# Performance work log

Hardware: AMD Instinct MI355X
Metric: run time of the kernel (lower is better)

Reference implementation:

```python
import jax, jax.numpy as jnp
import numpy as np

N = 500000
M = 8  # max vertices after clipping a 4-gon by 4 half-planes


def _angle_sort(q):
    # q: (4,2) points in convex position -> CCW-ordered convex quad (== convex hull)
    c = q.mean(axis=0)
    ang = jnp.arctan2(q[:, 1] - c[1], q[:, 0] - c[0])
    return q[jnp.argsort(ang)]


def _poly_inter_area(subj, clip):
    # Sutherland-Hodgman clipping of CCW convex quad `subj` by CCW convex quad `clip`.
    poly = jnp.zeros((M, 2), subj.dtype).at[:4].set(subj)
    n = jnp.array(4, jnp.int32)
    edges = jnp.stack([clip, jnp.roll(clip, -1, axis=0)], axis=1)  # (4,2,2)

    def clip_edge(state, edge):
        poly, n = state
        a, b = edge[0], edge[1]
        e = b - a
        idx = jnp.arange(M)
        n_safe = jnp.maximum(n, 1)
        nxt = poly[(idx + 1) % n_safe]
        d_cur = e[0] * (poly[:, 1] - a[1]) - e[1] * (poly[:, 0] - a[0])
        d_nxt = e[0] * (nxt[:, 1] - a[1]) - e[1] * (nxt[:, 0] - a[0])
        in_cur = d_cur >= 0
        in_nxt = d_nxt >= 0
        den = d_cur - d_nxt
        den = jnp.where(jnp.abs(den) < 1e-12, 1e-12, den)
        t = (d_cur / den)[:, None]
        ipt = poly + t * (nxt - poly)
        active = idx < n
        pts = jnp.stack([poly, ipt], axis=1).reshape(2 * M, 2)
        valid = jnp.stack([active & in_cur, active & (in_cur != in_nxt)], axis=1).reshape(2 * M)
        pos = jnp.cumsum(valid) - 1
        new_poly = jnp.zeros((M, 2), poly.dtype).at[jnp.where(valid, pos, M)].set(pts, mode='drop')
        return (new_poly, jnp.sum(valid).astype(jnp.int32)), None

    (poly, n), _ = jax.lax.scan(clip_edge, (poly, n), edges)
    idx = jnp.arange(M)
    n_safe = jnp.maximum(n, 1)
    nxtv = poly[(idx + 1) % n_safe]
    mask = (idx < n).astype(poly.dtype)
    return 0.5 * jnp.abs(jnp.sum(mask * (poly[:, 0] * nxtv[:, 1] - nxtv[:, 0] * poly[:, 1])))


def _hull_area8(pts):
    # Area of convex hull of 8 points via gift wrapping (fixed 8 steps, pads by repeating start).
    P = 8
    start = jnp.argmin(pts[:, 1]).astype(jnp.int32)

    def next_idx(cur):
        rel = pts - pts[cur]
        d2 = jnp.sum(rel * rel, axis=1)
        C = rel[:, 0, None] * rel[None, :, 1] - rel[:, 1, None] * rel[None, :, 0]  # C[j,k]=cross(rel_j, rel_k)
        valid = jnp.all(C >= -1e-6, axis=1) & (d2 > 1e-12)  # all points left of cur->j
        score = jnp.where(valid, d2, -1.0)
        return jnp.argmax(score).astype(jnp.int32)

    def step(carry, _):
        cur, done = carry
        nxt = next_idx(cur)
        nxt = jnp.where(done, cur, nxt)
        done = done | (nxt == start)
        return (nxt, done), nxt

    _, seq = jax.lax.scan(step, (start, jnp.array(False)), None, length=P)
    order = jnp.concatenate([start[None], seq])  # (9,)
    v = pts[order]
    x, y = v[:, 0], v[:, 1]
    xn, yn = jnp.roll(x, -1), jnp.roll(y, -1)
    return 0.5 * jnp.abs(jnp.sum(x * yn - xn * y))


def _pair_loss(pred8, tgt8):
    p = _angle_sort(pred8.reshape(4, 2))
    t = _angle_sort(tgt8.reshape(4, 2))
    inter = _poly_inter_area(p, t)
    hull = _hull_area8(jnp.concatenate([p, t], axis=0))  # convex hull of union of points
    iou = jnp.where(hull > 1e-12, inter / jnp.maximum(hull, 1e-12), 0.0)
    return 1.0 - iou  # reduction='none', loss_type='iou'


def setup_inputs() -> dict:
    key = jax.random.key(0)
    ks = jax.random.split(key, 6)

    def make_quads(ka, kb, kc):
        # 4 vertices in convex position: sorted angles + radius in [0.5, 1.5]
        ang = jnp.sort(jax.random.uniform(ka, (N, 4)) * (2.0 * np.pi), axis=1)
        rad = 0.5 + jax.random.uniform(kb, (N, 4))
        ctr = jax.random.normal(kc, (N, 1, 2)) * 0.5
        pts = ctr + jnp.stack([rad * jnp.cos(ang), rad * jnp.sin(ang)], axis=-1)
        return pts.reshape(N, 8).astype(jnp.float32)

    preds = make_quads(ks[0], ks[1], ks[2])
    targets = make_quads(ks[3], ks[4], ks[5])
    return {"preds": preds, "targets": targets}


def reference(preds, targets):
    return jax.vmap(_pair_loss)(preds, targets)
```

## Files before the change

### kernel.cpp

```cpp
#include <hip/hip_runtime.h>
#include <math.h>

struct V2 { float x, y; };

#define NT 256

__device__ __forceinline__ int ang_class(float x, float y) {
    return (y < 0.f) ? 0 : ((y > 0.f) ? 2 : ((x >= 0.f) ? 1 : 3));
}

__device__ __forceinline__ void angle_sort4(float4 lo, float4 hi, V2 out[4]) {
    V2 p[4];
    p[0].x = lo.x; p[0].y = lo.y;
    p[1].x = lo.z; p[1].y = lo.w;
    p[2].x = hi.x; p[2].y = hi.y;
    p[3].x = hi.z; p[3].y = hi.w;
    float cx = (((p[0].x + p[1].x) + p[2].x) + p[3].x) * 0.25f;
    float cy = (((p[0].y + p[1].y) + p[2].y) + p[3].y) * 0.25f;
    float rx[4], ry[4]; int cls[4];
#pragma unroll
    for (int i = 0; i < 4; i++) {
        rx[i] = p[i].x - cx; ry[i] = p[i].y - cy;
        cls[i] = ang_class(rx[i], ry[i]);
    }
    int rank[4] = {0, 0, 0, 0};
#pragma unroll
    for (int i = 0; i < 4; i++) {
#pragma unroll
        for (int j = i + 1; j < 4; j++) {
            int cd = cls[i] - cls[j];
            double cr = (double)rx[i] * (double)ry[j] - (double)ry[i] * (double)rx[j];
            bool gt = (cd > 0) || (cd == 0 && cr < 0.0);
            rank[i] += gt ? 1 : 0;
            rank[j] += gt ? 0 : 1;
        }
    }
#pragma unroll
    for (int k = 0; k < 4; k++) {
#pragma unroll
        for (int i = 0; i < 4; i++) {
            if (rank[i] == k) out[k] = p[i];
        }
    }
}

__device__ __forceinline__ int clip_mid(float2 (*buf)[NT], V2 A, V2 B,
                                        int nv, int tid)
{
    float ex = B.x - A.x, ey = B.y - A.y;
    V2 p[8]; float d[8];
#pragma unroll
    for (int s = 0; s < 8; s++) {
        float2 v = buf[s][tid];
        p[s].x = v.x; p[s].y = v.y;
        d[s] = ex * (v.y - A.y) - ey * (v.x - A.x);
    }
    int cnt = 0;
#pragma unroll
    for (int idx = 0; idx < 8; idx++) {
        V2 nx; float dn;
        if (idx == 7) {
            bool w = (nv == 8);
            nx.x = w ? p[0].x : p[7].x;
            nx.y = w ? p[0].y : p[7].y;
            dn   = w ? d[0]   : d[7];
        } else {
            bool w = ((idx + 1) == nv);
            nx.x = w ? p[0].x : p[idx + 1].x;
            nx.y = w ? p[0].y : p[idx + 1].y;
            dn   = w ? d[0]   : d[idx + 1];
        }
        bool active = idx < nv;
        bool in_cur = d[idx] >= 0.f;
        bool in_nxt = dn >= 0.f;
        float den = d[idx] - dn;
        den = (fabsf(den) < 1e-12f) ? 1e-12f : den;
        float t = __fdividef(d[idx], den);
        float ix = p[idx].x + t * (nx.x - p[idx].x);
        float iy = p[idx].y + t * (nx.y - p[idx].y);
        bool v0 = active && in_cur;
        bool v1 = active && (in_cur != in_nxt);
        if (v0 && cnt < 8) buf[cnt][tid] = make_float2(p[idx].x, p[idx].y);
        cnt += v0 ? 1 : 0;
        if (v1 && cnt < 8) buf[cnt][tid] = make_float2(ix, iy);
        cnt += v1 ? 1 : 0;
    }
    return cnt;
}

__device__ __forceinline__ float clip_final(const float2 (*buf)[NT], V2 A, V2 B,
                                            int nv, int tid)
{
    float ex = B.x - A.x, ey = B.y - A.y;
    V2 p[8]; float d[8];
#pragma unroll
    for (int s = 0; s < 8; s++) {
        float2 v = buf[s][tid];
        p[s].x = v.x; p[s].y = v.y;
        d[s] = ex * (v.y - A.y) - ey * (v.x - A.x);
    }
    int cnt = 0;
    float sx = 0.f;
    float fx = 0.f, fy = 0.f;
    float px = 0.f, py = 0.f;
#pragma unroll
    for (int idx = 0; idx < 8; idx++) {
        V2 nx; float dn;
        if (idx == 7) {
            bool w = (nv == 8);
            nx.x = w ? p[0].x : p[7].x;
            nx.y = w ? p[0].y : p[7].y;
            dn   = w ? d[0]   : d[7];
        } else {
            bool w = ((idx + 1) == nv);
            nx.x = w ? p[0].x : p[idx + 1].x;
            nx.y = w ? p[0].y : p[idx + 1].y;
            dn   = w ? d[0]   : d[idx + 1];
        }
        bool active = idx < nv;
        bool in_cur = d[idx] >= 0.f;
        bool in_nxt = dn >= 0.f;
        float den = d[idx] - dn;
        den = (fabsf(den) < 1e-12f) ? 1e-12f : den;
        float t = __fdividef(d[idx], den);
        float ix = p[idx].x + t * (nx.x - p[idx].x);
        float iy = p[idx].y + t * (nx.y - p[idx].y);
        bool v0 = active && in_cur;
        bool v1 = active && (in_cur != in_nxt);
        {
            bool w0 = (cnt == 0), wl = (cnt <= 7);
            float qx = p[idx].x, qy = p[idx].y;
            if (v0) {
                fx = w0 ? qx : fx; fy = w0 ? qy : fy;
                sx += (!w0 && wl) ? (px * qy - qx * py) : 0.f;
                px = wl ? qx : px; py = wl ? qy : py;
            }
            cnt += v0 ? 1 : 0;
        }
        {
            bool w0 = (cnt == 0), wl = (cnt <= 7);
            if (v1) {
                fx = w0 ? ix : fx; fy = w0 ? iy : fy;
                sx += (!w0 && wl) ? (px * iy - ix * py) : 0.f;
                px = wl ? ix : px; py = wl ? iy : py;
            }
            cnt += v1 ? 1 : 0;
        }
    }
    if (cnt > 0 && cnt <= 8) sx += px * fy - fx * py;
    return 0.5f * fabsf(sx);
}

__global__ __launch_bounds__(256, 8) void poly_iou_kernel(
    const float* __restrict__ preds, const float* __restrict__ targets,
    float* __restrict__ out, int n)
{
    __shared__ float2 buf[8][NT];
    int tid = threadIdx.x;
    int gid = blockIdx.x * NT + tid;
    if (gid >= n) return;

    const float4* p4 = reinterpret_cast<const float4*>(preds);
    const float4* t4 = reinterpret_cast<const float4*>(targets);
    float4 a0 = p4[2 * gid], a1 = p4[2 * gid + 1];
    float4 b0 = t4[2 * gid], b1 = t4[2 * gid + 1];

    V2 P[4], T[4];
    angle_sort4(a0, a1, P);
    angle_sort4(b0, b1, T);

    int nv;
    {
        float ex = T[1].x - T[0].x, ey = T[1].y - T[0].y;
        float dd[4];
#pragma unroll
        for (int k = 0; k < 4; k++)
            dd[k] = ex * (P[k].y - T[0].y) - ey * (P[k].x - T[0].x);
        int cnt = 0;
#pragma unroll
        for (int idx = 0; idx < 4; idx++) {
            int j = (idx + 1) & 3;
            bool in_cur = dd[idx] >= 0.f;
            bool in_nxt = dd[j] >= 0.f;
            float den = dd[idx] - dd[j];
            den = (fabsf(den) < 1e-12f) ? 1e-12f : den;
            float t = __fdividef(dd[idx], den);
            float ix = P[idx].x + t * (P[j].x - P[idx].x);
            float iy = P[idx].y + t * (P[j].y - P[idx].y);
            bool v1 = (in_cur != in_nxt);
            if (in_cur) buf[cnt][tid] = make_float2(P[idx].x, P[idx].y);
            cnt += in_cur ? 1 : 0;
            if (v1) buf[cnt][tid] = make_float2(ix, iy);
            cnt += v1 ? 1 : 0;
        }
        nv = cnt;
    }

    nv = clip_mid(buf, T[1], T[2], nv, tid);
    nv = clip_mid(buf, T[2], T[3], nv, tid);
    float inter = clip_final(buf, T[3], T[0], nv, tid);

    V2 h[8];
#pragma unroll
    for (int k = 0; k < 4; k++) { h[k] = P[k]; h[4 + k] = T[k]; }

    int start = 0; V2 vs = h[0];
#pragma unroll
    for (int k = 1; k < 8; k++) {
        bool b = h[k].y < vs.y;
        start = b ? k : start;
        vs.x  = b ? h[k].x : vs.x;
        vs.y  = b ? h[k].y : vs.y;
    }

    V2 pc = vs; int cur = start; bool done = false; float harea = 0.f;
#pragma unroll
    for (int s = 0; s < 8; s++) {
        int best = cur;
        float bx = 0.f, by = 0.f, bd = 0.f, px = pc.x, py = pc.y;
#pragma unroll
        for (int k = 0; k < 8; k++) {
            float rx = h[k].x - pc.x, ry = h[k].y - pc.y;
            float d2 = rx * rx + ry * ry;
            bool ok = d2 > 1e-12f;
            float c = bx * ry - by * rx;
            bool take = ok && ((c < 0.f) || ((c == 0.f) && (d2 > bd)));
            best = take ? k : best;
            bx = take ? rx : bx; by = take ? ry : by; bd = take ? d2 : bd;
            px = take ? h[k].x : px; py = take ? h[k].y : py;
        }
        int nxt = done ? cur : best;
        V2 pv;
        pv.x = done ? pc.x : px;
        pv.y = done ? pc.y : py;
        harea += pc.x * pv.y - pv.x * pc.y;
        done = done || (nxt == start);
        pc = pv; cur = nxt;
    }
    harea += pc.x * vs.y - vs.x * pc.y;
    harea = 0.5f * fabsf(harea);

    float iou = (harea > 1e-12f) ? (inter / fmaxf(harea, 1e-12f)) : 0.f;
    out[gid] = 1.f - iou;
}

extern "C" void kernel_launch(void* const* d_in, const int* in_sizes, int n_in,
                              void* d_out, int out_size, void* d_ws, size_t ws_size,
                              hipStream_t stream) {
    const float* preds = (const float*)d_in[0];
    const float* targets = (const float*)d_in[1];
    float* out = (float*)d_out;
    int n = in_sizes[0] / 8;
    int block = NT;
    int grid = (n + block - 1) / block;
    hipLaunchKernelGGL(poly_iou_kernel, dim3(grid), dim3(block), 0, stream,
                       preds, targets, out, n);
}
```

Baseline: 32.80 us.

## Use sorting network, branchless LDS stores, and tree reduction in gift wrapping

```diff
diff --git a/kernel.cpp b/kernel.cpp
--- a/kernel.cpp
+++ b/kernel.cpp
@@ -10,65 +10,58 @@
 }
 
 __device__ __forceinline__ void angle_sort4(float4 lo, float4 hi, V2 out[4]) {
-    V2 p[4];
-    p[0].x = lo.x; p[0].y = lo.y;
-    p[1].x = lo.z; p[1].y = lo.w;
-    p[2].x = hi.x; p[2].y = hi.y;
-    p[3].x = hi.z; p[3].y = hi.w;
-    float cx = (((p[0].x + p[1].x) + p[2].x) + p[3].x) * 0.25f;
-    float cy = (((p[0].y + p[1].y) + p[2].y) + p[3].y) * 0.25f;
-    float rx[4], ry[4]; int cls[4];
+    float x[4] = {lo.x, lo.z, hi.x, hi.z};
+    float y[4] = {lo.y, lo.w, hi.y, hi.w};
+    float cx = (((x[0] + x[1]) + x[2]) + x[3]) * 0.25f;
+    float cy = (((y[0] + y[1]) + y[2]) + y[3]) * 0.25f;
+    float rx[4], ry[4]; int cl[4];
 #pragma unroll
     for (int i = 0; i < 4; i++) {
-        rx[i] = p[i].x - cx; ry[i] = p[i].y - cy;
-        cls[i] = ang_class(rx[i], ry[i]);
-    }
-    int rank[4] = {0, 0, 0, 0};
-#pragma unroll
-    for (int i = 0; i < 4; i++) {
-#pragma unroll
-        for (int j = i + 1; j < 4; j++) {
-            int cd = cls[i] - cls[j];
-            double cr = (double)rx[i] * (double)ry[j] - (double)ry[i] * (double)rx[j];
-            bool gt = (cd > 0) || (cd == 0 && cr < 0.0);
-            rank[i] += gt ? 1 : 0;
-            rank[j] += gt ? 0 : 1;
-        }
-    }
-#pragma unroll
-    for (int k = 0; k < 4; k++) {
-#pragma unroll
-        for (int i = 0; i < 4; i++) {
-            if (rank[i] == k) out[k] = p[i];
-        }
-    }
+        rx[i] = x[i] - cx; ry[i] = y[i] - cy;
+        cl[i] = ang_class(rx[i], ry[i]);
+    }
+#define CE(i, j) { \
+    int cd = cl[i] - cl[j]; \
+    double cr = (double)rx[i] * (double)ry[j] - (double)ry[i] * (double)rx[j]; \
+    bool gt = (cd > 0) || (cd == 0 && cr < 0.0);   \
+    float t; int ti; \
+    t = x[i];  x[i]  = gt ? x[j]  : x[i];  x[j]  = gt ? t  : x[j]; \
+    t = y[i];  y[i]  = gt ? y[j]  : y[i];  y[j]  = gt ? t  : y[j]; \
+    t = rx[i]; rx[i] = gt ? rx[j] : rx[i]; rx[j] = gt ? t  : rx[j]; \
+    t = ry[i]; ry[i] = gt ? ry[j] : ry[i]; ry[j] = gt ? t  : ry[j]; \
+    ti = cl[i]; cl[i] = gt ? cl[j] : cl[i]; cl[j] = gt ? ti : cl[j]; \
+}
+    CE(0, 1) CE(2, 3) CE(0, 2) CE(1, 3) CE(1, 2)
+#undef CE
+#pragma unroll
+    for (int k = 0; k < 4; k++) { out[k].x = x[k]; out[k].y = y[k]; }
 }
 
 __device__ __forceinline__ int clip_mid(float2 (*buf)[NT], V2 A, V2 B,
                                         int nv, int tid)
 {
     float ex = B.x - A.x, ey = B.y - A.y;
-    V2 p[8]; float d[8];
+    float qx[8], qy[8], d[8];
 #pragma unroll
     for (int s = 0; s < 8; s++) {
         float2 v = buf[s][tid];
-        p[s].x = v.x; p[s].y = v.y;
+        qx[s] = v.x; qy[s] = v.y;
         d[s] = ex * (v.y - A.y) - ey * (v.x - A.x);
     }
     int cnt = 0;
 #pragma unroll
     for (int idx = 0; idx < 8; idx++) {
-        V2 nx; float dn;
+        float nxx, nxy, dn;
         if (idx == 7) {
             bool w = (nv == 8);
-            nx.x = w ? p[0].x : p[7].x;
-            nx.y = w ? p[0].y : p[7].y;
-            dn   = w ? d[0]   : d[7];
+            nxx = w ? qx[0] : qx[7];
+            nxy = w ? qy[0] : qy[7];
+            dn  = w ? d[0]  : d[7];
         } else {
             bool w = ((idx + 1) == nv);
-            nx.x = w ? p[0].x : p[idx + 1].x;
-            nx.y = w ? p[0].y : p[idx + 1].y;
-            dn   = w ? d[0]   : d[idx + 1];
+            nxx = w ? qx[0] : qx[idx + 1];
+            nxy = w ? qy[0] : qy[idx + 1];
+            dn  = w ? d[0]  : d[idx + 1];
         }
         bool active = idx < nv;
         bool in_cur = d[idx] >= 0.f;
@@ -76,13 +69,15 @@
         float den = d[idx] - dn;
         den = (fabsf(den) < 1e-12f) ? 1e-12f : den;
         float t = __fdividef(d[idx], den);
-        float ix = p[idx].x + t * (nx.x - p[idx].x);
-        float iy = p[idx].y + t * (nx.y - p[idx].y);
+        float ix = qx[idx] + t * (nxx - qx[idx]);
+        float iy = qy[idx] + t * (nxy - qy[idx]);
         bool v0 = active && in_cur;
         bool v1 = active && (in_cur != in_nxt);
-        if (v0 && cnt < 8) buf[cnt][tid] = make_float2(p[idx].x, p[idx].y);
+        int s0 = (v0 && cnt < 8) ? cnt : 8;
+        buf[s0][tid] = make_float2(qx[idx], qy[idx]);
         cnt += v0 ? 1 : 0;
-        if (v1 && cnt < 8) buf[cnt][tid] = make_float2(ix, iy);
+        int s1 = (v1 && cnt < 8) ? cnt : 8;
+        buf[s1][tid] = make_float2(ix, iy);
         cnt += v1 ? 1 : 0;
     }
     return cnt;
@@ -92,11 +87,11 @@
                                             int nv, int tid)
 {
     float ex = B.x - A.x, ey = B.y - A.y;
-    V2 p[8]; float d[8];
+    float qx[8], qy[8], d[8];
 #pragma unroll
     for (int s = 0; s < 8; s++) {
         float2 v = buf[s][tid];
-        p[s].x = v.x; p[s].y = v.y;
+        qx[s] = v.x; qy[s] = v.y;
         d[s] = ex * (v.y - A.y) - ey * (v.x - A.x);
     }
     int cnt = 0;
@@ -105,17 +100,17 @@
     float px = 0.f, py = 0.f;
 #pragma unroll
     for (int idx = 0; idx < 8; idx++) {
-        V2 nx; float dn;
+        float nxx, nxy, dn;
         if (idx == 7) {
             bool w = (nv == 8);
-            nx.x = w ? p[0].x : p[7].x;
-            nx.y = w ? p[0].y : p[7].y;
-            dn   = w ? d[0]   : d[7];
+            nxx = w ? qx[0] : qx[7];
+            nxy = w ? qy[0] : qy[7];
+            dn  = w ? d[0]  : d[7];
         } else {
             bool w = ((idx + 1) == nv);
-            nx.x = w ? p[0].x : p[idx + 1].x;
-            nx.y = w ? p[0].y : p[idx + 1].y;
-            dn   = w ? d[0]   : d[idx + 1];
+            nxx = w ? qx[0] : qx[idx + 1];
+            nxy = w ? qy[0] : qy[idx + 1];
+            dn  = w ? d[0]  : d[idx + 1];
         }
         bool active = idx < nv;
         bool in_cur = d[idx] >= 0.f;
@@ -123,17 +118,16 @@
         float den = d[idx] - dn;
         den = (fabsf(den) < 1e-12f) ? 1e-12f : den;
         float t = __fdividef(d[idx], den);
-        float ix = p[idx].x + t * (nx.x - p[idx].x);
-        float iy = p[idx].y + t * (nx.y - p[idx].y);
+        float ix = qx[idx] + t * (nxx - qx[idx]);
+        float iy = qy[idx] + t * (nxy - qy[idx]);
         bool v0 = active && in_cur;
         bool v1 = active && (in_cur != in_nxt);
         {
             bool w0 = (cnt == 0), wl = (cnt <= 7);
-            float qx = p[idx].x, qy = p[idx].y;
             if (v0) {
-                fx = w0 ? qx : fx; fy = w0 ? qy : fy;
-                sx += (!w0 && wl) ? (px * qy - qx * py) : 0.f;
-                px = wl ? qx : px; py = wl ? qy : py;
+                fx = w0 ? qx[idx] : fx; fy = w0 ? qy[idx] : fy;
+                sx += (!w0 && wl) ? (px * qy[idx] - qx[idx] * py) : 0.f;
+                px = wl ? qx[idx] : px; py = wl ? qy[idx] : py;
             }
             cnt += v0 ? 1 : 0;
         }
@@ -151,11 +145,22 @@
     return 0.5f * fabsf(sx);
 }
 
+struct Cand { float rx, ry, d2, px, py; };
+
+__device__ __forceinline__ Cand mcw(Cand a, Cand b) {
+    float c = a.rx * b.ry - a.ry * b.rx;
+    bool tb = (b.d2 > 0.f) && ((c < 0.f) || ((c == 0.f) && (b.d2 > a.d2)));
+    Cand o;
+    o.rx = tb ? b.rx : a.rx; o.ry = tb ? b.ry : a.ry; o.d2 = tb ? b.d2 : a.d2;
+    o.px = tb ? b.px : a.px; o.py = tb ? b.py : a.py;
+    return o;
+}
+
 __global__ __launch_bounds__(256, 8) void poly_iou_kernel(
     const float* __restrict__ preds, const float* __restrict__ targets,
     float* __restrict__ out, int n)
 {
-    __shared__ float2 buf[8][NT];
+    __shared__ float2 buf[9][NT];
     int tid = threadIdx.x;
     int gid = blockIdx.x * NT + tid;
     if (gid >= n) return;
@@ -188,9 +193,11 @@
             float ix = P[idx].x + t * (P[j].x - P[idx].x);
             float iy = P[idx].y + t * (P[j].y - P[idx].y);
             bool v1 = (in_cur != in_nxt);
-            if (in_cur) buf[cnt][tid] = make_float2(P[idx].x, P[idx].y);
+            int s0 = in_cur ? cnt : 8;
+            buf[s0][tid] = make_float2(P[idx].x, P[idx].y);
             cnt += in_cur ? 1 : 0;
-            if (v1) buf[cnt][tid] = make_float2(ix, iy);
+            int s1 = v1 ? cnt : 8;
+            buf[s1][tid] = make_float2(ix, iy);
             cnt += v1 ? 1 : 0;
         }
         nv = cnt;
@@ -200,44 +207,50 @@
     nv = clip_mid(buf, T[2], T[3], nv, tid);
     float inter = clip_final(buf, T[3], T[0], nv, tid);
 
-    V2 h[8];
-#pragma unroll
-    for (int k = 0; k < 4; k++) { h[k] = P[k]; h[4 + k] = T[k]; }
-
-    int start = 0; V2 vs = h[0];
+    float hx[8], hy[8];
+#pragma unroll
+    for (int k = 0; k < 4; k++) {
+        hx[k] = P[k].x; hy[k] = P[k].y;
+        hx[4 + k] = T[k].x; hy[4 + k] = T[k].y;
+    }
+
+    float vsx = hx[0], vsy = hy[0];
 #pragma unroll
     for (int k = 1; k < 8; k++) {
-        bool b = h[k].y < vs.y;
-        start = b ? k : start;
-        vs.x  = b ? h[k].x : vs.x;
-        vs.y  = b ? h[k].y : vs.y;
-    }
-
-    V2 pc = vs; int cur = start; bool done = false; float harea = 0.f;
+        bool b = hy[k] < vsy;
+        vsx = b ? hx[k] : vsx;
+        vsy = b ? hy[k] : vsy;
+    }
+
+    float pcx = vsx, pcy = vsy;
+    bool done = false;
+    float harea = 0.f;
 #pragma unroll
     for (int s = 0; s < 8; s++) {
-        int best = cur;
-        float bx = 0.f, by = 0.f, bd = 0.f, px = pc.x, py = pc.y;
+        Cand c[8];
 #pragma unroll
         for (int k = 0; k < 8; k++) {
-            float rx = h[k].x - pc.x, ry = h[k].y - pc.y;
-            float d2 = rx * rx + ry * ry;
-            bool ok = d2 > 1e-12f;
-            float c = bx * ry - by * rx;
-            bool take = ok && ((c < 0.f) || ((c == 0.f) && (d2 > bd)));
-            best = take ? k : best;
-            bx = take ? rx : bx; by = take ? ry : by; bd = take ? d2 : bd;
-            px = take ? h[k].x : px; py = take ? h[k].y : py;
-        }
-        int nxt = done ? cur : best;
-        V2 pv;
-        pv.x = done ? pc.x : px;
-        pv.y = done ? pc.y : py;
-        harea += pc.x * pv.y - pv.x * pc.y;
-        done = done || (nxt == start);
-        pc = pv; cur = nxt;
-    }
-    harea += pc.x * vs.y - vs.x * pc.y;
+            float ux = hx[k] - pcx, uy = hy[k] - pcy;
+            float dd = ux * ux + uy * uy;
+            bool ok = dd > 1e-12f;
+            c[k].rx = ok ? ux : 0.f;
+            c[k].ry = ok ? uy : 0.f;
+            c[k].d2 = ok ? dd : -1.f;
+            c[k].px = hx[k]; c[k].py = hy[k];
+        }
+        Cand w01 = mcw(c[0], c[1]), w23 = mcw(c[2], c[3]);
+        Cand w45 = mcw(c[4], c[5]), w67 = mcw(c[6], c[7]);
+        Cand wA = mcw(w01, w23), wB = mcw(w45, w67);
+        Cand w = mcw(wA, wB);
+
+        bool stay = done || (w.d2 < 0.f);
+        float pvx = stay ? pcx : w.px;
+        float pvy = stay ? pcy : w.py;
+        harea += pcx * pvy - pvx * pcy;
+        done = done || ((pvx == vsx) && (pvy == vsy));
+        pcx = pvx; pcy = pvy;
+    }
+    harea += pcx * vsy - vsx * pcy;
     harea = 0.5f * fabsf(harea);
 
     float iou = (harea > 1e-12f) ? (inter / fmaxf(harea, 1e-12f)) : 0.f;
```

New measurement: 41.45 us. 26.4% more time.
